# Kernel optimization log

Measured on AMD Instinct MI355X. Metric: run time of the kernel, lower is better.

## Reference

```python
import jax, jax.numpy as jnp
import numpy as np

N_NODES = 100000


def _spmm(edge_src, edge_dst, edge_vals, support):
    # out[i] = sum_{e: dst(e)=i} w_e * support[src(e)]  (sparse adj @ support)
    msgs = support[edge_src] * edge_vals[:, None]  # [E, F]
    return jax.ops.segment_sum(msgs, edge_dst, num_segments=N_NODES)


def setup_inputs() -> dict:
    key = jax.random.key(0)
    ks = jax.random.split(key, 8)
    E = 1600000
    feat_dim, nhid, num_class = 256, 64, 16
    x = jax.random.normal(ks[0], (N_NODES, feat_dim), dtype=jnp.float32)
    edge_src = jax.random.randint(ks[1], (E,), 0, N_NODES, dtype=jnp.int32)
    edge_dst = jax.random.randint(ks[2], (E,), 0, N_NODES, dtype=jnp.int32)
    edge_vals = jax.random.uniform(ks[3], (E,), dtype=jnp.float32)
    # Glorot-style init as in the original GraphConvolution.reset_parameters
    W1 = jax.random.normal(ks[4], (feat_dim, nhid), dtype=jnp.float32) / np.sqrt(feat_dim)
    b1 = jnp.zeros((nhid,), dtype=jnp.float32)
    W2 = jax.random.normal(ks[5], (nhid, num_class), dtype=jnp.float32) / np.sqrt(nhid)
    b2 = jnp.zeros((num_class,), dtype=jnp.float32)
    return {"x": x, "edge_src": edge_src, "edge_dst": edge_dst,
            "edge_vals": edge_vals, "W1": W1, "b1": b1, "W2": W2, "b2": b2}


def reference(x, edge_src, edge_dst, edge_vals, W1, b1, W2, b2):
    # gc1: support = x @ W1 ; out = adj @ support + b1 ; relu
    h = jax.nn.relu(_spmm(edge_src, edge_dst, edge_vals, x @ W1) + b1)
    # dropout is identity in eval mode (training=False)
    # gc2
    logits = _spmm(edge_src, edge_dst, edge_vals, h @ W2) + b2
    return jax.nn.log_softmax(logits, axis=1)
```

## Files before the change

### kernel.cpp

```cpp
#include <hip/hip_runtime.h>
#include <hip/hip_fp16.h>

#define N_NODES 100000
#define E_EDGES 1600000
#define F_IN    256
#define F_HID   64
#define F_OUT   16
#define NBKT    391
#define CAP     4608
#define GEMM1_BLOCKS 782
#define PA_BLOCKS    782

typedef _Float16 half8   __attribute__((ext_vector_type(8)));
typedef float    floatx4 __attribute__((ext_vector_type(4)));

__global__ __launch_bounds__(256) void gemm1_kernel(const float* __restrict__ x,
                                                    const float* __restrict__ W1,
                                                    _Float16* __restrict__ support1) {
    __shared__ __align__(16) _Float16 Bs[16384];
    const int t = threadIdx.x;
    for (int i = t; i < 16384; i += 256) {
        const int k = i >> 6, n = i & 63;
        const int kb = k >> 5, quad = (k >> 3) & 3, j = k & 7;
        const int nt = n >> 4, ln = n & 15;
        Bs[((kb * 4 + nt) * 64 + quad * 16 + ln) * 8 + j] = (_Float16)W1[i];
    }
    __syncthreads();

    const int wave = t >> 6;
    const int lane = t & 63;
    const int ln   = lane & 15;
    const int quad = lane >> 4;
    const int row0 = blockIdx.x * 128 + wave * 32;

    const float* xp[2];
#pragma unroll
    for (int mt = 0; mt < 2; ++mt) {
        int r = row0 + mt * 16 + ln;
        if (r > N_NODES - 1) r = N_NODES - 1;
        xp[mt] = x + (size_t)r * F_IN + quad * 8;
    }

    floatx4 acc[2][4] = {};

#pragma unroll 4
    for (int kb = 0; kb < 8; ++kb) {
        half8 a[2];
#pragma unroll
        for (int mt = 0; mt < 2; ++mt) {
            float4 v0 = *(const float4*)(xp[mt] + kb * 32);
            float4 v1 = *(const float4*)(xp[mt] + kb * 32 + 4);
            half8 h;
            h[0] = (_Float16)v0.x; h[1] = (_Float16)v0.y;
            h[2] = (_Float16)v0.z; h[3] = (_Float16)v0.w;
            h[4] = (_Float16)v1.x; h[5] = (_Float16)v1.y;
            h[6] = (_Float16)v1.z; h[7] = (_Float16)v1.w;
            a[mt] = h;
        }
#pragma unroll
        for (int nt = 0; nt < 4; ++nt) {
            half8 b = *(const half8*)&Bs[((size_t)((kb * 4 + nt) * 64 + lane)) * 8];
            acc[0][nt] = __builtin_amdgcn_mfma_f32_16x16x32_f16(a[0], b, acc[0][nt], 0, 0, 0);
            acc[1][nt] = __builtin_amdgcn_mfma_f32_16x16x32_f16(a[1], b, acc[1][nt], 0, 0, 0);
        }
    }

#pragma unroll
    for (int mt = 0; mt < 2; ++mt) {
        const int rbase = row0 + mt * 16 + quad * 4;
#pragma unroll
        for (int r = 0; r < 4; ++r) {
            const int row = rbase + r;
            if (row < N_NODES) {
#pragma unroll
                for (int nt = 0; nt < 4; ++nt)
                    support1[(size_t)row * F_HID + nt * 16 + ln] = (_Float16)acc[mt][nt][r];
            }
        }
    }
}

__global__ __launch_bounds__(256) void passA_kernel(const int* __restrict__ esrc,
                                                    const int* __restrict__ edst,
                                                    const float* __restrict__ evals,
                                                    int* __restrict__ bucketCursor,
                                                    int2* __restrict__ tmp) {
    __shared__ int hist[NBKT];
    __shared__ int base[NBKT];
    const int t = threadIdx.x;
    for (int i = t; i < NBKT; i += 256) hist[i] = 0;
    __syncthreads();
    const int base_e = blockIdx.x * 2048;
    int rks[2][4];
#pragma unroll
    for (int ch = 0; ch < 2; ++ch) {
        const int e0 = base_e + ch * 1024 + t * 4;
        if (e0 < E_EDGES) {
            int4 d4 = *(const int4*)&edst[e0];
            rks[ch][0] = atomicAdd(&hist[d4.x >> 8], 1);
            rks[ch][1] = atomicAdd(&hist[d4.y >> 8], 1);
            rks[ch][2] = atomicAdd(&hist[d4.z >> 8], 1);
            rks[ch][3] = atomicAdd(&hist[d4.w >> 8], 1);
        }
    }
    __syncthreads();
    for (int i = t; i < NBKT; i += 256) {
        const int h = hist[i];
        if (h) base[i] = atomicAdd(&bucketCursor[i], h);
    }
    __syncthreads();
#pragma unroll
    for (int ch = 0; ch < 2; ++ch) {
        const int e0 = base_e + ch * 1024 + t * 4;
        if (e0 < E_EDGES) {
            int4 d4 = *(const int4*)&edst[e0];
            int4 s4 = *(const int4*)&esrc[e0];
            float4 v4 = *(const float4*)&evals[e0];
            const int dd[4] = {d4.x, d4.y, d4.z, d4.w};
            const int ss[4] = {s4.x, s4.y, s4.z, s4.w};
            const float vv[4] = {v4.x, v4.y, v4.z, v4.w};
#pragma unroll
            for (int u = 0; u < 4; ++u) {
                const int bu = dd[u] >> 8;
                const int bpos = base[bu] + rks[ch][u];
                if (bpos < CAP)
                    tmp[(size_t)bu * CAP + bpos] =
                        make_int2(((dd[u] & 255) << 17) | ss[u],
                                  __float_as_int(vv[u]));
            }
        }
    }
}

__global__ __launch_bounds__(256) void passB_kernel(const int2* __restrict__ tmp,
                                                    const int* __restrict__ bucketCursor,
                                                    int2* __restrict__ sorted_edges,
                                                    int* __restrict__ rowstart,
                                                    int* __restrict__ deg) {
    __shared__ int ldeg[256];
    __shared__ int lcur[256];
    __shared__ int s[256];
    const int t = threadIdx.x;
    const int b = blockIdx.x;
    const int beg = b * CAP;
    int cnt = bucketCursor[b];
    if (cnt > CAP) cnt = CAP;

    ldeg[t] = 0;
    __syncthreads();

    for (int p = t; p < cnt; p += 256) {
        int2 r = tmp[beg + p];
        atomicAdd(&ldeg[r.x >> 17], 1);
    }
    __syncthreads();

    const int v = ldeg[t];
    s[t] = v;
    __syncthreads();
#pragma unroll
    for (int off = 1; off < 256; off <<= 1) {
        const int y = (t >= off) ? s[t - off] : 0;
        __syncthreads();
        s[t] += y;
        __syncthreads();
    }
    const int run = s[t] - v;
    lcur[t] = run;
    const int node = b * 256 + t;
    if (node < N_NODES) { rowstart[node] = beg + run; deg[node] = v; }
    __syncthreads();

    for (int p = t; p < cnt; p += 256) {
        int2 r = tmp[beg + p];
        const int pos = beg + atomicAdd(&lcur[r.x >> 17], 1);
        sorted_edges[pos] = make_int2(r.x & 0x1FFFF, r.y);
    }
}

__global__ __launch_bounds__(256) void spmm1_fused_kernel(const int* __restrict__ rowstart,
                                                          const int* __restrict__ deg,
                                                          const int2* __restrict__ sorted_edges,
                                                          const _Float16* __restrict__ support1,
                                                          const float* __restrict__ b1,
                                                          const float* __restrict__ W2,
                                                          _Float16* __restrict__ support2) {
    __shared__ float W2s[64 * 17];
    __shared__ float b1s[64];
    __shared__ __align__(16) float hs[4][64];
    const int t = threadIdx.x;
    for (int i = t; i < 1024; i += 256)
        W2s[(i >> 4) * 17 + (i & 15)] = W2[i];
    if (t < 64) b1s[t] = b1[t];
    __syncthreads();

    const int wave = t >> 6;
    const int lane = t & 63;
    const int node = blockIdx.x * 4 + wave;
    const int c4 = lane & 15;
    const int q  = lane >> 4;

    const int beg = rowstart[node];
    const int cnt = deg[node];

    int   src_l = 0;
    float val_l = 0.f;
    if (lane < cnt) {
        int2 ev = sorted_edges[beg + lane];
        src_l = ev.x;
        val_l = __int_as_float(ev.y);
    }

    float acc0 = 0.f, acc1 = 0.f, acc2 = 0.f, acc3 = 0.f;
    const int kmax  = cnt < 64 ? cnt : 64;
    const int quads = (kmax + 3) >> 2;
    const int qp    = (quads + 3) & ~3;
    for (int k = 0; k < qp; k += 4) {
        float w[4]; uint2 d[4];
#pragma unroll
        for (int u = 0; u < 4; ++u) {
            const int idx = 4 * (k + u) + q;
            const int s2  = __shfl(src_l, idx);
            w[u] = __shfl(val_l, idx);
            d[u] = *(const uint2*)&support1[(size_t)s2 * F_HID + 4 * c4];
        }
#pragma unroll
        for (int u = 0; u < 4; ++u) {
            const _Float16* hp = (const _Float16*)&d[u];
            acc0 = fmaf(w[u], (float)hp[0], acc0);
            acc1 = fmaf(w[u], (float)hp[1], acc1);
            acc2 = fmaf(w[u], (float)hp[2], acc2);
            acc3 = fmaf(w[u], (float)hp[3], acc3);
        }
    }
    for (int k = 64 + q; k < cnt; k += 4) {
        int2 ev = sorted_edges[beg + k];
        const float w = __int_as_float(ev.y);
        const uint2 d = *(const uint2*)&support1[(size_t)ev.x * F_HID + 4 * c4];
        const _Float16* hp = (const _Float16*)&d;
        acc0 = fmaf(w, (float)hp[0], acc0);
        acc1 = fmaf(w, (float)hp[1], acc1);
        acc2 = fmaf(w, (float)hp[2], acc2);
        acc3 = fmaf(w, (float)hp[3], acc3);
    }

    acc0 += __shfl_xor(acc0, 16); acc0 += __shfl_xor(acc0, 32);
    acc1 += __shfl_xor(acc1, 16); acc1 += __shfl_xor(acc1, 32);
    acc2 += __shfl_xor(acc2, 16); acc2 += __shfl_xor(acc2, 32);
    acc3 += __shfl_xor(acc3, 16); acc3 += __shfl_xor(acc3, 32);
    if (q == 0) {
        float4 hv;
        hv.x = fmaxf(acc0 + b1s[4 * c4],     0.f);
        hv.y = fmaxf(acc1 + b1s[4 * c4 + 1], 0.f);
        hv.z = fmaxf(acc2 + b1s[4 * c4 + 2], 0.f);
        hv.w = fmaxf(acc3 + b1s[4 * c4 + 3], 0.f);
        *(float4*)&hs[wave][4 * c4] = hv;
    }
    __syncthreads();

    const int ln   = lane & 15;
    const int quad = lane >> 4;
    float o = 0.f;
#pragma unroll
    for (int kk = 0; kk < 16; ++kk) {
        const int k2 = quad * 16 + kk;
        o = fmaf(hs[wave][k2], W2s[k2 * 17 + ln], o);
    }
    o += __shfl_xor(o, 16);
    o += __shfl_xor(o, 32);
    if (quad == 0)
        support2[(size_t)node * F_OUT + ln] = (_Float16)o;
}

__global__ __launch_bounds__(256) void spmm2_fused_kernel(const int* __restrict__ rowstart,
                                                          const int* __restrict__ deg,
                                                          const int2* __restrict__ sorted_edges,
                                                          const _Float16* __restrict__ support2,
                                                          const float* __restrict__ b2,
                                                          float* __restrict__ out) {
    __shared__ float b2s[16];
    const int t = threadIdx.x;
    if (t < 16) b2s[t] = b2[t];
    __syncthreads();

    const int j    = t & 15;
    const int node = blockIdx.x * 16 + (t >> 4);
    const int c = j & 3;
    const int p = j >> 2;

    const int beg = rowstart[node];
    const int cnt = deg[node];

    int   src_a = 0, src_b = 0;
    float val_a = 0.f, val_b = 0.f;
    if (j < cnt)      { int2 ev = sorted_edges[beg + j];      src_a = ev.x; val_a = __int_as_float(ev.y); }
    if (j + 16 < cnt) { int2 ev = sorted_edges[beg + 16 + j]; src_b = ev.x; val_b = __int_as_float(ev.y); }

    float acc0 = 0.f, acc1 = 0.f, acc2 = 0.f, acc3 = 0.f;
    {
        float w[4]; uint2 d[4];
#pragma unroll
        for (int u = 0; u < 4; ++u) {
            const int idx = 4 * u + p;
            const int s2  = __shfl(src_a, idx, 16);
            w[u] = __shfl(val_a, idx, 16);
            d[u] = *(const uint2*)&support2[(size_t)s2 * F_OUT + 4 * c];
        }
#pragma unroll
        for (int u = 0; u < 4; ++u) {
            const _Float16* hp = (const _Float16*)&d[u];
            acc0 = fmaf(w[u], (float)hp[0], acc0);
            acc1 = fmaf(w[u], (float)hp[1], acc1);
            acc2 = fmaf(w[u], (float)hp[2], acc2);
            acc3 = fmaf(w[u], (float)hp[3], acc3);
        }
    }
    if (cnt > 16) {
        float w[4]; uint2 d[4];
#pragma unroll
        for (int u = 0; u < 4; ++u) {
            const int idx = 4 * u + p;
            const int s2  = __shfl(src_b, idx, 16);
            w[u] = __shfl(val_b, idx, 16);
            d[u] = *(const uint2*)&support2[(size_t)s2 * F_OUT + 4 * c];
        }
#pragma unroll
        for (int u = 0; u < 4; ++u) {
            const _Float16* hp = (const _Float16*)&d[u];
            acc0 = fmaf(w[u], (float)hp[0], acc0);
            acc1 = fmaf(w[u], (float)hp[1], acc1);
            acc2 = fmaf(w[u], (float)hp[2], acc2);
            acc3 = fmaf(w[u], (float)hp[3], acc3);
        }
    }
    for (int k = 32 + p; k < cnt; k += 4) {
        int2 ev = sorted_edges[beg + k];
        const float w = __int_as_float(ev.y);
        const uint2 d = *(const uint2*)&support2[(size_t)ev.x * F_OUT + 4 * c];
        const _Float16* hp = (const _Float16*)&d;
        acc0 = fmaf(w, (float)hp[0], acc0);
        acc1 = fmaf(w, (float)hp[1], acc1);
        acc2 = fmaf(w, (float)hp[2], acc2);
        acc3 = fmaf(w, (float)hp[3], acc3);
    }

    acc0 += __shfl_xor(acc0, 4, 16); acc0 += __shfl_xor(acc0, 8, 16);
    acc1 += __shfl_xor(acc1, 4, 16); acc1 += __shfl_xor(acc1, 8, 16);
    acc2 += __shfl_xor(acc2, 4, 16); acc2 += __shfl_xor(acc2, 8, 16);
    acc3 += __shfl_xor(acc3, 4, 16); acc3 += __shfl_xor(acc3, 8, 16);

    const float v0 = acc0 + b2s[4 * c];
    const float v1 = acc1 + b2s[4 * c + 1];
    const float v2 = acc2 + b2s[4 * c + 2];
    const float v3 = acc3 + b2s[4 * c + 3];
    float m = fmaxf(fmaxf(v0, v1), fmaxf(v2, v3));
    m = fmaxf(m, __shfl_xor(m, 1, 16));
    m = fmaxf(m, __shfl_xor(m, 2, 16));
    float sum = __expf(v0 - m) + __expf(v1 - m) + __expf(v2 - m) + __expf(v3 - m);
    sum += __shfl_xor(sum, 1, 16);
    sum += __shfl_xor(sum, 2, 16);
    if (p == 0) {
        const float lse = m + __logf(sum);
        float4 o = make_float4(v0 - lse, v1 - lse, v2 - lse, v3 - lse);
        *(float4*)&out[(size_t)node * F_OUT + 4 * c] = o;
    }
}

extern "C" void kernel_launch(void* const* d_in, const int* in_sizes, int n_in,
                              void* d_out, int out_size, void* d_ws, size_t ws_size,
                              hipStream_t stream) {
    const float* x     = (const float*)d_in[0];
    const int*   esrc  = (const int*)  d_in[1];
    const int*   edst  = (const int*)  d_in[2];
    const float* evals = (const float*)d_in[3];
    const float* W1    = (const float*)d_in[4];
    const float* b1    = (const float*)d_in[5];
    const float* W2    = (const float*)d_in[6];
    const float* b2    = (const float*)d_in[7];
    float* out = (float*)d_out;

    char* ws = (char*)d_ws;
    _Float16* support1     = (_Float16*)(ws);
    _Float16* support2     = (_Float16*)(ws + 12800000);
    int2*     tmp          = (int2*)    (ws + 16000000);
    int2*     sorted_edges = (int2*)    (ws + 30413824);
    int*      rowstart     = (int*)     (ws + 44827648);
    int*      deg          = (int*)     (ws + 45227648);
    int*      bucketCursor = (int*)     (ws + 45627648);

    hipMemsetAsync(bucketCursor, 0, NBKT * sizeof(int), stream);
    gemm1_kernel<<<GEMM1_BLOCKS, 256, 0, stream>>>(x, W1, support1);
    passA_kernel<<<PA_BLOCKS, 256, 0, stream>>>(esrc, edst, evals, bucketCursor, tmp);
    passB_kernel<<<NBKT, 256, 0, stream>>>(tmp, bucketCursor, sorted_edges, rowstart, deg);
    spmm1_fused_kernel<<<N_NODES / 4, 256, 0, stream>>>(rowstart, deg, sorted_edges,
                                                        support1, b1, W2, support2);
    spmm2_fused_kernel<<<N_NODES / 16, 256, 0, stream>>>(rowstart, deg, sorted_edges,
                                                         support2, b2, out);
}
```

Baseline: 313.0 us.

## Merge GEMM1 with edge bucketing pass and use packed fp16 accumulation in SpMM

Converts W1 to fp16 in a small prep kernel, which also zeroes the bucket cursors and so replaces the memset. The GEMM1 kernel and the edge-bucketing pass A are merged into one launch whose block index picks the role, so the two independent phases run concurrently and per-block LDS staging of W1 is dropped. Both SpMM kernels now accumulate in packed half2 with fp16 weights and use 32-bit shift indexing instead of size_t multiplies. Accumulating sums of up to dozens of terms in fp16 reduces accuracy and risks tolerance failures. W1 operands are now read from global memory instead of LDS.

After: 285.5 us. -8.8%, faster.

```diff
diff --git a/kernel.cpp b/kernel.cpp
--- a/kernel.cpp
+++ b/kernel.cpp
@@ -12,20 +12,78 @@
 #define PA_BLOCKS    782
 
 typedef _Float16 half8   __attribute__((ext_vector_type(8)));
+typedef _Float16 half2v  __attribute__((ext_vector_type(2)));
 typedef float    floatx4 __attribute__((ext_vector_type(4)));
 
-__global__ __launch_bounds__(256) void gemm1_kernel(const float* __restrict__ x,
-                                                    const float* __restrict__ W1,
-                                                    _Float16* __restrict__ support1) {
-    __shared__ __align__(16) _Float16 Bs[16384];
+__global__ __launch_bounds__(256) void prep_kernel(const float* __restrict__ W1,
+                                                   _Float16* __restrict__ W1h,
+                                                   int* __restrict__ bucketCursor) {
+    const int i = blockIdx.x * 256 + threadIdx.x;
+    if (i < NBKT) bucketCursor[i] = 0;
+    const int k = i >> 6, n = i & 63;
+    const int kb = k >> 5, quad = (k >> 3) & 3, j = k & 7;
+    const int nt = n >> 4, ln = n & 15;
+    W1h[((kb * 4 + nt) * 64 + quad * 16 + ln) * 8 + j] = (_Float16)W1[i];
+}
+
+__global__ __launch_bounds__(256) void gemm1_passA_kernel(const float* __restrict__ x,
+                                                          const _Float16* __restrict__ W1h,
+                                                          _Float16* __restrict__ support1,
+                                                          const int* __restrict__ esrc,
+                                                          const int* __restrict__ edst,
+                                                          const float* __restrict__ evals,
+                                                          int* __restrict__ bucketCursor,
+                                                          int2* __restrict__ tmp) {
+    __shared__ int hist[NBKT];
+    __shared__ int base[NBKT];
     const int t = threadIdx.x;
-    for (int i = t; i < 16384; i += 256) {
-        const int k = i >> 6, n = i & 63;
-        const int kb = k >> 5, quad = (k >> 3) & 3, j = k & 7;
-        const int nt = n >> 4, ln = n & 15;
-        Bs[((kb * 4 + nt) * 64 + quad * 16 + ln) * 8 + j] = (_Float16)W1[i];
-    }
-    __syncthreads();
+
+    if (blockIdx.x >= GEMM1_BLOCKS) {
+        const int blk = blockIdx.x - GEMM1_BLOCKS;
+        for (int i = t; i < NBKT; i += 256) hist[i] = 0;
+        __syncthreads();
+        const int base_e = blk * 2048;
+        int rks[2][4];
+#pragma unroll
+        for (int ch = 0; ch < 2; ++ch) {
+            const int e0 = base_e + ch * 1024 + t * 4;
+            if (e0 < E_EDGES) {
+                int4 d4 = *(const int4*)&edst[e0];
+                rks[ch][0] = atomicAdd(&hist[d4.x >> 8], 1);
+                rks[ch][1] = atomicAdd(&hist[d4.y >> 8], 1);
+                rks[ch][2] = atomicAdd(&hist[d4.z >> 8], 1);
+                rks[ch][3] = atomicAdd(&hist[d4.w >> 8], 1);
+            }
+        }
+        __syncthreads();
+        for (int i = t; i < NBKT; i += 256) {
+            const int h = hist[i];
+            if (h) base[i] = atomicAdd(&bucketCursor[i], h);
+        }
+        __syncthreads();
+#pragma unroll
+        for (int ch = 0; ch < 2; ++ch) {
+            const int e0 = base_e + ch * 1024 + t * 4;
+            if (e0 < E_EDGES) {
+                int4 d4 = *(const int4*)&edst[e0];
+                int4 s4 = *(const int4*)&esrc[e0];
+                float4 v4 = *(const float4*)&evals[e0];
+                const int dd[4] = {d4.x, d4.y, d4.z, d4.w};
+                const int ss[4] = {s4.x, s4.y, s4.z, s4.w};
+                const float vv[4] = {v4.x, v4.y, v4.z, v4.w};
+#pragma unroll
+                for (int u = 0; u < 4; ++u) {
+                    const int bu = dd[u] >> 8;
+                    const int bpos = base[bu] + rks[ch][u];
+                    if (bpos < CAP)
+                        tmp[(size_t)bu * CAP + bpos] =
+                            make_int2(((dd[u] & 255) << 17) | ss[u],
+                                      __float_as_int(vv[u]));
+                }
+            }
+        }
+        return;
+    }
 
     const int wave = t >> 6;
     const int lane = t & 63;
@@ -59,7 +117,7 @@
         }
 #pragma unroll
         for (int nt = 0; nt < 4; ++nt) {
-            half8 b = *(const half8*)&Bs[((size_t)((kb * 4 + nt) * 64 + lane)) * 8];
+            half8 b = *(const half8*)&W1h[((size_t)((kb * 4 + nt) * 64 + lane)) * 8];
             acc[0][nt] = __builtin_amdgcn_mfma_f32_16x16x32_f16(a[0], b, acc[0][nt], 0, 0, 0);
             acc[1][nt] = __builtin_amdgcn_mfma_f32_16x16x32_f16(a[1], b, acc[1][nt], 0, 0, 0);
         }
@@ -75,58 +133,6 @@
 #pragma unroll
                 for (int nt = 0; nt < 4; ++nt)
                     support1[(size_t)row * F_HID + nt * 16 + ln] = (_Float16)acc[mt][nt][r];
-            }
-        }
-    }
-}
-
-__global__ __launch_bounds__(256) void passA_kernel(const int* __restrict__ esrc,
-                                                    const int* __restrict__ edst,
-                                                    const float* __restrict__ evals,
-                                                    int* __restrict__ bucketCursor,
-                                                    int2* __restrict__ tmp) {
-    __shared__ int hist[NBKT];
-    __shared__ int base[NBKT];
-    const int t = threadIdx.x;
-    for (int i = t; i < NBKT; i += 256) hist[i] = 0;
-    __syncthreads();
-    const int base_e = blockIdx.x * 2048;
-    int rks[2][4];
-#pragma unroll
-    for (int ch = 0; ch < 2; ++ch) {
-        const int e0 = base_e + ch * 1024 + t * 4;
-        if (e0 < E_EDGES) {
-            int4 d4 = *(const int4*)&edst[e0];
-            rks[ch][0] = atomicAdd(&hist[d4.x >> 8], 1);
-            rks[ch][1] = atomicAdd(&hist[d4.y >> 8], 1);
-            rks[ch][2] = atomicAdd(&hist[d4.z >> 8], 1);
-            rks[ch][3] = atomicAdd(&hist[d4.w >> 8], 1);
-        }
-    }
-    __syncthreads();
-    for (int i = t; i < NBKT; i += 256) {
-        const int h = hist[i];
-        if (h) base[i] = atomicAdd(&bucketCursor[i], h);
-    }
-    __syncthreads();
-#pragma unroll
-    for (int ch = 0; ch < 2; ++ch) {
-        const int e0 = base_e + ch * 1024 + t * 4;
-        if (e0 < E_EDGES) {
-            int4 d4 = *(const int4*)&edst[e0];
-            int4 s4 = *(const int4*)&esrc[e0];
-            float4 v4 = *(const float4*)&evals[e0];
-            const int dd[4] = {d4.x, d4.y, d4.z, d4.w};
-            const int ss[4] = {s4.x, s4.y, s4.z, s4.w};
-            const float vv[4] = {v4.x, v4.y, v4.z, v4.w};
-#pragma unroll
-            for (int u = 0; u < 4; ++u) {
-                const int bu = dd[u] >> 8;
-                const int bpos = base[bu] + rks[ch][u];
-                if (bpos < CAP)
-                    tmp[(size_t)bu * CAP + bpos] =
-                        make_int2(((dd[u] & 255) << 17) | ss[u],
-                                  __float_as_int(vv[u]));
             }
         }
     }
@@ -211,7 +217,8 @@
         val_l = __int_as_float(ev.y);
     }
 
-    float acc0 = 0.f, acc1 = 0.f, acc2 = 0.f, acc3 = 0.f;
+    half2v a01 = {(_Float16)0, (_Float16)0};
+    half2v a23 = {(_Float16)0, (_Float16)0};
     const int kmax  = cnt < 64 ? cnt : 64;
     const int quads = (kmax + 3) >> 2;
     const int qp    = (quads + 3) & ~3;
@@ -222,28 +229,29 @@
             const int idx = 4 * (k + u) + q;
             const int s2  = __shfl(src_l, idx);
             w[u] = __shfl(val_l, idx);
-            d[u] = *(const uint2*)&support1[(size_t)s2 * F_HID + 4 * c4];
-        }
-#pragma unroll
-        for (int u = 0; u < 4; ++u) {
-            const _Float16* hp = (const _Float16*)&d[u];
-            acc0 = fmaf(w[u], (float)hp[0], acc0);
-            acc1 = fmaf(w[u], (float)hp[1], acc1);
-            acc2 = fmaf(w[u], (float)hp[2], acc2);
-            acc3 = fmaf(w[u], (float)hp[3], acc3);
+            d[u] = *(const uint2*)&support1[(s2 << 6) + 4 * c4];
+        }
+#pragma unroll
+        for (int u = 0; u < 4; ++u) {
+            const half2v* hp = (const half2v*)&d[u];
+            const _Float16 wh = (_Float16)w[u];
+            const half2v w2 = {wh, wh};
+            a01 += w2 * hp[0];
+            a23 += w2 * hp[1];
         }
     }
     for (int k = 64 + q; k < cnt; k += 4) {
         int2 ev = sorted_edges[beg + k];
-        const float w = __int_as_float(ev.y);
-        const uint2 d = *(const uint2*)&support1[(size_t)ev.x * F_HID + 4 * c4];
-        const _Float16* hp = (const _Float16*)&d;
-        acc0 = fmaf(w, (float)hp[0], acc0);
-        acc1 = fmaf(w, (float)hp[1], acc1);
-        acc2 = fmaf(w, (float)hp[2], acc2);
-        acc3 = fmaf(w, (float)hp[3], acc3);
-    }
-
+        const uint2 d = *(const uint2*)&support1[(ev.x << 6) + 4 * c4];
+        const half2v* hp = (const half2v*)&d;
+        const _Float16 wh = (_Float16)__int_as_float(ev.y);
+        const half2v w2 = {wh, wh};
+        a01 += w2 * hp[0];
+        a23 += w2 * hp[1];
+    }
+
+    float acc0 = (float)a01[0], acc1 = (float)a01[1];
+    float acc2 = (float)a23[0], acc3 = (float)a23[1];
     acc0 += __shfl_xor(acc0, 16); acc0 += __shfl_xor(acc0, 32);
     acc1 += __shfl_xor(acc1, 16); acc1 += __shfl_xor(acc1, 32);
     acc2 += __shfl_xor(acc2, 16); acc2 += __shfl_xor(acc2, 32);
@@ -296,7 +304,8 @@
     if (j < cnt)      { int2 ev = sorted_edges[beg + j];      src_a = ev.x; val_a = __int_as_float(ev.y); }
     if (j + 16 < cnt) { int2 ev = sorted_edges[beg + 16 + j]; src_b = ev.x; val_b = __int_as_float(ev.y); }
 
-    float acc0 = 0.f, acc1 = 0.f, acc2 = 0.f, acc3 = 0.f;
+    half2v a01 = {(_Float16)0, (_Float16)0};
+    half2v a23 = {(_Float16)0, (_Float16)0};
     {
         float w[4]; uint2 d[4];
 #pragma unroll
@@ -304,15 +313,15 @@
             const int idx = 4 * u + p;
             const int s2  = __shfl(src_a, idx, 16);
             w[u] = __shfl(val_a, idx, 16);
-            d[u] = *(const uint2*)&support2[(size_t)s2 * F_OUT + 4 * c];
-        }
-#pragma unroll
-        for (int u = 0; u < 4; ++u) {
-            const _Float16* hp = (const _Float16*)&d[u];
-            acc0 = fmaf(w[u], (float)hp[0], acc0);
-            acc1 = fmaf(w[u], (float)hp[1], acc1);
-            acc2 = fmaf(w[u], (float)hp[2], acc2);
-            acc3 = fmaf(w[u], (float)hp[3], acc3);
+            d[u] = *(const uint2*)&support2[(s2 << 4) + 4 * c];
+        }
+#pragma unroll
+        for (int u = 0; u < 4; ++u) {
+            const half2v* hp = (const half2v*)&d[u];
+            const _Float16 wh = (_Float16)w[u];
+            const half2v w2 = {wh, wh};
+            a01 += w2 * hp[0];
+            a23 += w2 * hp[1];
         }
     }
     if (cnt > 16) {
@@ -322,28 +331,29 @@
             const int idx = 4 * u + p;
             const int s2  = __shfl(src_b, idx, 16);
             w[u] = __shfl(val_b, idx, 16);
-            d[u] = *(const uint2*)&support2[(size_t)s2 * F_OUT + 4 * c];
-        }
-#pragma unroll
-        for (int u = 0; u < 4; ++u) {
-            const _Float16* hp = (const _Float16*)&d[u];
-            acc0 = fmaf(w[u], (float)hp[0], acc0);
-            acc1 = fmaf(w[u], (float)hp[1], acc1);
-            acc2 = fmaf(w[u], (float)hp[2], acc2);
-            acc3 = fmaf(w[u], (float)hp[3], acc3);
+            d[u] = *(const uint2*)&support2[(s2 << 4) + 4 * c];
+        }
+#pragma unroll
+        for (int u = 0; u < 4; ++u) {
+            const half2v* hp = (const half2v*)&d[u];
+            const _Float16 wh = (_Float16)w[u];
+            const half2v w2 = {wh, wh};
+            a01 += w2 * hp[0];
+            a23 += w2 * hp[1];
         }
     }
     for (int k = 32 + p; k < cnt; k += 4) {
         int2 ev = sorted_edges[beg + k];
-        const float w = __int_as_float(ev.y);
-        const uint2 d = *(const uint2*)&support2[(size_t)ev.x * F_OUT + 4 * c];
-        const _Float16* hp = (const _Float16*)&d;
-        acc0 = fmaf(w, (float)hp[0], acc0);
-        acc1 = fmaf(w, (float)hp[1], acc1);
-        acc2 = fmaf(w, (float)hp[2], acc2);
-        acc3 = fmaf(w, (float)hp[3], acc3);
-    }
-
+        const uint2 d = *(const uint2*)&support2[(ev.x << 4) + 4 * c];
+        const half2v* hp = (const half2v*)&d;
+        const _Float16 wh = (_Float16)__int_as_float(ev.y);
+        const half2v w2 = {wh, wh};
+        a01 += w2 * hp[0];
+        a23 += w2 * hp[1];
+    }
+
+    float acc0 = (float)a01[0], acc1 = (float)a01[1];
+    float acc2 = (float)a23[0], acc3 = (float)a23[1];
     acc0 += __shfl_xor(acc0, 4, 16); acc0 += __shfl_xor(acc0, 8, 16);
     acc1 += __shfl_xor(acc1, 4, 16); acc1 += __shfl_xor(acc1, 8, 16);
     acc2 += __shfl_xor(acc2, 4, 16); acc2 += __shfl_xor(acc2, 8, 16);
@@ -387,10 +397,11 @@
     int*      rowstart     = (int*)     (ws + 44827648);
     int*      deg          = (int*)     (ws + 45227648);
     int*      bucketCursor = (int*)     (ws + 45627648);
-
-    hipMemsetAsync(bucketCursor, 0, NBKT * sizeof(int), stream);
-    gemm1_kernel<<<GEMM1_BLOCKS, 256, 0, stream>>>(x, W1, support1);
-    passA_kernel<<<PA_BLOCKS, 256, 0, stream>>>(esrc, edst, evals, bucketCursor, tmp);
+    _Float16* W1h          = (_Float16*)(ws + 45629216);
+
+    prep_kernel<<<64, 256, 0, stream>>>(W1, W1h, bucketCursor);
+    gemm1_passA_kernel<<<GEMM1_BLOCKS + PA_BLOCKS, 256, 0, stream>>>(
+        x, W1h, support1, esrc, edst, evals, bucketCursor, tmp);
     passB_kernel<<<NBKT, 256, 0, stream>>>(tmp, bucketCursor, sorted_edges, rowstart, deg);
     spmm1_fused_kernel<<<N_NODES / 4, 256, 0, stream>>>(rowstart, deg, sorted_edges,
                                                         support1, b1, W2, support2);
```
